# Kernel tuning notes

Hardware: AMD Instinct MI355X
Metric: run time of the kernel (lower is better)

Reference implementation:

```python
import jax, jax.numpy as jnp
import numpy as np

B, T, C = 4, 4096, 256

def setup_inputs() -> dict:
    key = jax.random.key(0)
    ks = jax.random.split(key, 7)
    s = 1.0 / np.sqrt(C)
    return {
        "x": jax.random.normal(ks[0], (B, T, C), dtype=jnp.float32),
        "Wq": jax.random.uniform(ks[1], (C, C), jnp.float32, -s, s),
        "bq": jax.random.uniform(ks[2], (C,), jnp.float32, -s, s),
        "Wk": jax.random.uniform(ks[3], (C, C), jnp.float32, -s, s),
        "bk": jax.random.uniform(ks[4], (C,), jnp.float32, -s, s),
        "Wv": jax.random.uniform(ks[5], (C, C), jnp.float32, -s, s),
        "bv": jax.random.uniform(ks[6], (C,), jnp.float32, -s, s),
    }

def reference(x, Wq, bq, Wk, bk, Wv, bv):
    # Projections (torch Linear: y = x @ W^T + b; here W stored as [in,out])
    q = x @ Wq + bq  # [B,T,C]
    k = x @ Wk + bk
    v = x @ Wv + bv
    dk = q.shape[-1]
    scores = jnp.einsum('btc,bsc->bts', q, k) / jnp.sqrt(jnp.float32(dk))
    Tn = x.shape[1]
    causal = jnp.tril(jnp.ones((Tn, Tn), dtype=bool))  # [T,T]
    scores = jnp.where(causal[None, :, :], scores, jnp.float32(-1e9))
    attn = jax.nn.softmax(scores, axis=-1)
    return jnp.einsum('bts,bsc->btc', attn, v)
```

## Files before the change

### kernel.cpp

```cpp
#include <hip/hip_runtime.h>
#include <hip/hip_bf16.h>

#define T_SEQ 4096
#define DIM   256
#define NBATCH 4

typedef short s8v __attribute__((ext_vector_type(8)));
typedef float f4v __attribute__((ext_vector_type(4)));
typedef unsigned short u16;

#define MFMA16(a,b,c) __builtin_amdgcn_mfma_f32_16x16x32_bf16(a,b,c,0,0,0)
#define FENCE_LGKM() asm volatile("s_waitcnt lgkmcnt(0)" ::: "memory")

__device__ int g_cnt[4];

static __device__ __forceinline__ u16 f2bf(float f) {
  union { float f; unsigned int u; } c; c.f = f;
  unsigned int u = c.u;
  unsigned int r = (u + 0x7fffu + ((u >> 16) & 1u)) >> 16;
  return (u16)r;
}

static __device__ __forceinline__ s8v pack8(const float* p) {
  float4 a = *(const float4*)p;
  float4 b = *(const float4*)(p + 4);
  s8v r;
  r[0] = (short)f2bf(a.x); r[1] = (short)f2bf(a.y);
  r[2] = (short)f2bf(a.z); r[3] = (short)f2bf(a.w);
  r[4] = (short)f2bf(b.x); r[5] = (short)f2bf(b.y);
  r[6] = (short)f2bf(b.z); r[7] = (short)f2bf(b.w);
  return r;
}

__global__ void diag_fill_kernel(float* __restrict__ out, float val, int n) {
  int i = blockIdx.x * blockDim.x + threadIdx.x;
  if (i < n) out[i] = val;
}

__global__ void wtrans_kernel(const float* __restrict__ Wq, const float* __restrict__ Wk,
                              const float* __restrict__ Wv, u16* __restrict__ Wt) {
  if (blockIdx.x == 0 && blockIdx.y == 0 && blockIdx.z == 0 &&
      threadIdx.y == 0 && threadIdx.x < 4)
    g_cnt[threadIdx.x] = 0;
  __shared__ float tile[32][33];
  int m = blockIdx.z;
  const float* W = (m == 0) ? Wq : ((m == 1) ? Wk : Wv);
  int bx = blockIdx.x * 32, by = blockIdx.y * 32;
  int x = threadIdx.x, y = threadIdx.y;
  #pragma unroll
  for (int i = 0; i < 32; i += 8) tile[y + i][x] = W[(by + y + i) * DIM + bx + x];
  __syncthreads();
  u16* o = Wt + m * DIM * DIM;
  #pragma unroll
  for (int i = 0; i < 32; i += 8) o[(bx + y + i) * DIM + by + x] = f2bf(tile[x][y + i]);
}

__global__ __launch_bounds__(256) void proj_kernel(
    const float* __restrict__ x, const u16* __restrict__ Wt,
    const float* __restrict__ bk, const float* __restrict__ bv,
    u16* __restrict__ kf, u16* __restrict__ vf) {
  alignas(16) __shared__ u16 Kl[64 * 264];
  alignas(16) __shared__ u16 Vl[256 * 72];

  int bid = blockIdx.x;
  int which = blockIdx.y;
  int tid  = threadIdx.x;
  int wave = tid >> 6, lane = tid & 63, quad = lane >> 4, l16 = lane & 15;
  int row0 = bid * 64 + wave * 16;

  s8v a[8];
  const float* xp = x + (size_t)(row0 + l16) * DIM + quad * 8;
  #pragma unroll
  for (int ks = 0; ks < 8; ks++) a[ks] = pack8(xp + ks * 32);

  if (which == 0) {
    const u16* W = Wt + DIM * DIM;
    f4v acc[16];
    #pragma unroll
    for (int nt = 0; nt < 16; nt++) acc[nt] = (f4v){0.f, 0.f, 0.f, 0.f};
    #pragma unroll
    for (int ks = 0; ks < 8; ks++) {
      #pragma unroll
      for (int nt = 0; nt < 16; nt++) {
        s8v bfr = *(const s8v*)(W + (nt * 16 + l16) * DIM + ks * 32 + quad * 8);
        acc[nt] = MFMA16(a[ks], bfr, acc[nt]);
      }
    }
    #pragma unroll
    for (int nt = 0; nt < 16; nt++) {
      float bb = bk[nt * 16 + l16];
      #pragma unroll
      for (int r = 0; r < 4; r++)
        Kl[(wave * 16 + quad * 4 + r) * 264 + nt * 16 + l16] = f2bf(acc[nt][r] + bb);
    }
    __syncthreads();
    #pragma unroll
    for (int i = 0; i < 8; i++) {
      int o = tid + i * 256;
      int tile = o >> 10, rem = o & 1023;
      int f = rem >> 6, ln = rem & 63;
      int sl = tile * 32 + (f >> 3) * 16 + (ln & 15);
      int c  = (f & 7) * 32 + (ln >> 4) * 8;
      s8v v = *(const s8v*)&Kl[sl * 264 + c];
      *(s8v*)&kf[(((size_t)(bid * 2 + tile) * 16 + f) * 64 + ln) * 8] = v;
    }
  } else {
    const u16* W = Wt + 2 * DIM * DIM;
    f4v acc[16];
    #pragma unroll
    for (int nt = 0; nt < 16; nt++) acc[nt] = (f4v){0.f, 0.f, 0.f, 0.f};
    #pragma unroll
    for (int ks = 0; ks < 8; ks++) {
      #pragma unroll
      for (int nt = 0; nt < 16; nt++) {
        s8v bfr = *(const s8v*)(W + (nt * 16 + l16) * DIM + ks * 32 + quad * 8);
        acc[nt] = MFMA16(a[ks], bfr, acc[nt]);
      }
    }
    #pragma unroll
    for (int nt = 0; nt < 16; nt++) {
      float bb = bv[nt * 16 + l16];
      union { u16 h[4]; uint2 v2; } pk;
      #pragma unroll
      for (int r = 0; r < 4; r++) pk.h[r] = f2bf(acc[nt][r] + bb);
      *(uint2*)&Vl[(nt * 16 + l16) * 72 + wave * 16 + quad * 4] = pk.v2;
    }
    __syncthreads();
    #pragma unroll
    for (int i = 0; i < 8; i++) {
      int o = tid + i * 256;
      int tile = o >> 10, rem = o & 1023;
      int nt = rem >> 6, ln = rem & 63;
      int c  = nt * 16 + (ln & 15);
      int sl = tile * 32 + (ln >> 4) * 8;
      s8v v = *(const s8v*)&Vl[c * 72 + sl];
      *(s8v*)&vf[(((size_t)(bid * 2 + tile) * 16 + nt) * 64 + ln) * 8] = v;
    }
  }
}

__global__ __launch_bounds__(256, 2) void attn_kernel(
    const float* __restrict__ x, const u16* __restrict__ wtq, const float* __restrict__ bq,
    const u16* __restrict__ kf, const u16* __restrict__ vf, float* __restrict__ out) {
  alignas(16) __shared__ u16 Qs[16 * 264];
  alignas(16) __shared__ float ObA[16 * 258];
  alignas(16) __shared__ float ObB[16 * 258];
  alignas(16) __shared__ u16 Ps[4 * 640];
  __shared__ float lbuf[4][16];
  __shared__ int taskS;

  int bid = blockIdx.x;
  int b = bid & 3;
  int tid = threadIdx.x;
  int wave = tid >> 6, lane = tid & 63, quad = lane >> 4, l16 = lane & 15;

  const u16* kfb = kf + (size_t)b * 128 * 8192;
  const u16* vfb = vf + (size_t)b * 128 * 8192;

  for (;;) {
    if (tid == 0) taskS = atomicAdd(&g_cnt[b], 1);
    __syncthreads();
    int t = taskS;
    if (t >= 256) break;
    int q = 255 - t;
    int row0 = q * 16;

    {
      s8v xa[8];
      const float* xp = x + (size_t)(b * T_SEQ + row0 + l16) * DIM + quad * 8;
      #pragma unroll
      for (int ks = 0; ks < 8; ks++) xa[ks] = pack8(xp + ks * 32);
      f4v qacc[4];
      #pragma unroll
      for (int j = 0; j < 4; j++) qacc[j] = (f4v){0.f, 0.f, 0.f, 0.f};
      #pragma unroll
      for (int ks = 0; ks < 8; ks++) {
        #pragma unroll
        for (int j = 0; j < 4; j++) {
          int nt = wave * 4 + j;
          s8v bfr = *(const s8v*)(wtq + (nt * 16 + l16) * DIM + ks * 32 + quad * 8);
          qacc[j] = MFMA16(xa[ks], bfr, qacc[j]);
        }
      }
      #pragma unroll
      for (int j = 0; j < 4; j++) {
        int nt = wave * 4 + j;
        float bb = bq[nt * 16 + l16];
        #pragma unroll
        for (int r = 0; r < 4; r++)
          Qs[(quad * 4 + r) * 264 + nt * 16 + l16] =
              f2bf((qacc[j][r] + bb) * 0.0625f);
      }
    }
    __syncthreads();
    s8v qa[8];
    #pragma unroll
    for (int ks = 0; ks < 8; ks++)
      qa[ks] = *(const s8v*)&Qs[l16 * 264 + ks * 32 + quad * 8];

    int n = (q >> 1) + 1;
    int lo = (n * wave) >> 2, hi = (n * (wave + 1)) >> 2;

    f4v o[16];
    #pragma unroll
    for (int nt = 0; nt < 16; nt++) o[nt] = (f4v){0.f, 0.f, 0.f, 0.f};
    float lrow[4] = {0.f, 0.f, 0.f, 0.f};

    #pragma unroll 1
    for (int kv = lo; kv < hi; kv++) {
      const u16* kt = kfb + (size_t)kv * 8192;
      const u16* vt = vfb + (size_t)kv * 8192;
      s8v kfr0[8], kfr1[8];
      #pragma unroll
      for (int f = 0; f < 8; f++) kfr0[f] = *(const s8v*)(kt + (f * 64 + lane) * 8);
      #pragma unroll
      for (int f = 0; f < 8; f++) kfr1[f] = *(const s8v*)(kt + ((8 + f) * 64 + lane) * 8);

      f4v c0 = (f4v){0.f, 0.f, 0.f, 0.f}, c1 = (f4v){0.f, 0.f, 0.f, 0.f};
      #pragma unroll
      for (int ks = 0; ks < 8; ks++) c0 = MFMA16(qa[ks], kfr0[ks], c0);
      s8v vfr0[8];
      #pragma unroll
      for (int f = 0; f < 8; f++) vfr0[f] = *(const s8v*)(vt + (f * 64 + lane) * 8);
      #pragma unroll
      for (int ks = 0; ks < 8; ks++) c1 = MFMA16(qa[ks], kfr1[ks], c1);
      s8v vfr1[8];
      #pragma unroll
      for (int f = 0; f < 8; f++) vfr1[f] = *(const s8v*)(vt + ((8 + f) * 64 + lane) * 8);

      int s0 = kv * 32 + l16;
      #pragma unroll
      for (int r = 0; r < 4; r++) {
        int tq = row0 + quad * 4 + r;
        float v0 = (s0 > tq)      ? -1e30f : c0[r];
        float v1 = (s0 + 16 > tq) ? -1e30f : c1[r];
        float p0 = __expf(v0);
        float p1 = __expf(v1);
        Ps[wave * 640 + (quad * 4 + r) * 40 + l16]      = f2bf(p0);
        Ps[wave * 640 + (quad * 4 + r) * 40 + 16 + l16] = f2bf(p1);
        lrow[r] += p0 + p1;
      }
      FENCE_LGKM();
      s8v pa = *(const s8v*)&Ps[wave * 640 + l16 * 40 + quad * 8];
      #pragma unroll
      for (int nt = 0; nt < 8; nt++) o[nt] = MFMA16(pa, vfr0[nt], o[nt]);
      #pragma unroll
      for (int nt = 0; nt < 8; nt++) o[8 + nt] = MFMA16(pa, vfr1[nt], o[8 + nt]);
    }

    #pragma unroll
    for (int r = 0; r < 4; r++) {
      #pragma unroll
      for (int d = 1; d < 16; d <<= 1) lrow[r] += __shfl_xor(lrow[r], d);
    }
    if (l16 == 0) {
      #pragma unroll
      for (int r = 0; r < 4; r++) lbuf[wave][quad * 4 + r] = lrow[r];
    }

    float* Obw = (wave & 1) ? ObB : ObA;
    if (wave < 2) {
      #pragma unroll
      for (int nt = 0; nt < 16; nt++) {
        #pragma unroll
        for (int r = 0; r < 4; r++)
          Obw[(quad * 4 + r) * 258 + nt * 16 + l16] = o[nt][r];
      }
    }
    __syncthreads();
    if (wave >= 2) {
      #pragma unroll
      for (int nt = 0; nt < 16; nt++) {
        #pragma unroll
        for (int r = 0; r < 4; r++)
          Obw[(quad * 4 + r) * 258 + nt * 16 + l16] += o[nt][r];
      }
    }
    __syncthreads();
    #pragma unroll
    for (int row = 0; row < 16; row++) {
      float s = lbuf[0][row] + lbuf[1][row] + lbuf[2][row] + lbuf[3][row];
      out[((size_t)(b * T_SEQ + row0 + row)) * DIM + tid] =
          (ObA[row * 258 + tid] + ObB[row * 258 + tid]) * (1.0f / s);
    }
  }
}

extern "C" void kernel_launch(void* const* d_in, const int* in_sizes, int n_in,
                              void* d_out, int out_size, void* d_ws, size_t ws_size,
                              hipStream_t stream) {
  const float* x  = (const float*)d_in[0];
  const float* Wq = (const float*)d_in[1];
  const float* bq = (const float*)d_in[2];
  const float* Wk = (const float*)d_in[3];
  const float* bk = (const float*)d_in[4];
  const float* Wv = (const float*)d_in[5];
  const float* bv = (const float*)d_in[6];

  const size_t NTD = (size_t)NBATCH * T_SEQ * DIM;
  const size_t WT_ELEMS = (size_t)3 * DIM * DIM;
  const size_t REQ_BYTES = (WT_ELEMS + 2 * NTD) * sizeof(u16);

  if (ws_size < REQ_BYTES) {
    float val = (float)(ws_size >> 20);
    diag_fill_kernel<<<(out_size + 255) / 256, 256, 0, stream>>>((float*)d_out, val, out_size);
    return;
  }

  u16* ws = (u16*)d_ws;
  u16* WT = ws;
  u16* Kf = ws + WT_ELEMS;
  u16* Vf = Kf + NTD;

  wtrans_kernel<<<dim3(8, 8, 3), dim3(32, 8, 1), 0, stream>>>(Wq, Wk, Wv, WT);
  proj_kernel<<<dim3(256, 2, 1), dim3(256, 1, 1), 0, stream>>>(x, WT, bk, bv, Kf, Vf);
  attn_kernel<<<dim3(512, 1, 1), dim3(256, 1, 1), 0, stream>>>(x, WT, bq, Kf, Vf, (float*)d_out);
}
```

Baseline: 220.8 us.

## Share K/V tiles in LDS across waves and split KV range with atomic accumulation

```diff
diff --git a/kernel.cpp b/kernel.cpp
--- a/kernel.cpp
+++ b/kernel.cpp
@@ -139,20 +139,27 @@
   }
 }
 
+__global__ void zero_kernel(float* __restrict__ out, float* __restrict__ lsum,
+                            int nOut, int nL) {
+  int i = blockIdx.x * blockDim.x + threadIdx.x;
+  int stride = gridDim.x * blockDim.x;
+  for (int k = i; k < nOut; k += stride) out[k] = 0.f;
+  for (int k = i; k < nL; k += stride) lsum[k] = 0.f;
+}
+
 __global__ __launch_bounds__(256, 2) void attn_kernel(
     const float* __restrict__ x, const u16* __restrict__ wtq, const float* __restrict__ bq,
-    const u16* __restrict__ kf, const u16* __restrict__ vf, float* __restrict__ out) {
-  alignas(16) __shared__ u16 Qs[16 * 264];
-  alignas(16) __shared__ float ObA[16 * 258];
-  alignas(16) __shared__ float ObB[16 * 258];
+    const u16* __restrict__ kf, const u16* __restrict__ vf,
+    float* __restrict__ lsum, float* __restrict__ out) {
+  alignas(16) __shared__ u16 KV[2][16384];
   alignas(16) __shared__ u16 Ps[4 * 640];
-  __shared__ float lbuf[4][16];
   __shared__ int taskS;
+  u16* Qs = &KV[0][0];
 
   int bid = blockIdx.x;
   int b = bid & 3;
   int tid = threadIdx.x;
-  int wave = tid >> 6, lane = tid & 63, quad = lane >> 4, l16 = lane & 15;
+  int w = tid >> 6, lane = tid & 63, quad = lane >> 4, l16 = lane & 15;
 
   const u16* kfb = kf + (size_t)b * 128 * 8192;
   const u16* vfb = vf + (size_t)b * 128 * 8192;
@@ -162,90 +169,140 @@
     __syncthreads();
     int t = taskS;
     if (t >= 256) break;
-    int q = 255 - t;
-    int row0 = q * 16;
+    int q64 = 63 - (t >> 2);
+    int qi  = t & 3;
+    int row0 = q64 * 64;
+    int n = 2 * q64 + 2;
+    int lo = (n * qi) >> 2, hi = (n * (qi + 1)) >> 2;
+    if (lo >= hi) continue;
 
     {
-      s8v xa[8];
-      const float* xp = x + (size_t)(b * T_SEQ + row0 + l16) * DIM + quad * 8;
-      #pragma unroll
-      for (int ks = 0; ks < 8; ks++) xa[ks] = pack8(xp + ks * 32);
-      f4v qacc[4];
-      #pragma unroll
-      for (int j = 0; j < 4; j++) qacc[j] = (f4v){0.f, 0.f, 0.f, 0.f};
+      f4v qacc[4][4];
+      #pragma unroll
+      for (int g = 0; g < 4; g++)
+        #pragma unroll
+        for (int j = 0; j < 4; j++) qacc[g][j] = (f4v){0.f, 0.f, 0.f, 0.f};
       #pragma unroll
       for (int ks = 0; ks < 8; ks++) {
-        #pragma unroll
-        for (int j = 0; j < 4; j++) {
-          int nt = wave * 4 + j;
-          s8v bfr = *(const s8v*)(wtq + (nt * 16 + l16) * DIM + ks * 32 + quad * 8);
-          qacc[j] = MFMA16(xa[ks], bfr, qacc[j]);
+        s8v wf[4];
+        #pragma unroll
+        for (int j = 0; j < 4; j++)
+          wf[j] = *(const s8v*)(wtq + ((w * 4 + j) * 16 + l16) * DIM + ks * 32 + quad * 8);
+        #pragma unroll
+        for (int g = 0; g < 4; g++) {
+          s8v xa = pack8(x + (size_t)(b * T_SEQ + row0 + g * 16 + l16) * DIM + ks * 32 + quad * 8);
+          #pragma unroll
+          for (int j = 0; j < 4; j++) qacc[g][j] = MFMA16(xa, wf[j], qacc[g][j]);
         }
       }
       #pragma unroll
       for (int j = 0; j < 4; j++) {
-        int nt = wave * 4 + j;
+        int nt = w * 4 + j;
         float bb = bq[nt * 16 + l16];
         #pragma unroll
-        for (int r = 0; r < 4; r++)
-          Qs[(quad * 4 + r) * 264 + nt * 16 + l16] =
-              f2bf((qacc[j][r] + bb) * 0.0625f);
+        for (int g = 0; g < 4; g++)
+          #pragma unroll
+          for (int r = 0; r < 4; r++)
+            Qs[(g * 16 + quad * 4 + r) * 264 + nt * 16 + l16] =
+                f2bf((qacc[g][j][r] + bb) * 0.0625f);
       }
     }
     __syncthreads();
     s8v qa[8];
     #pragma unroll
     for (int ks = 0; ks < 8; ks++)
-      qa[ks] = *(const s8v*)&Qs[l16 * 264 + ks * 32 + quad * 8];
-
-    int n = (q >> 1) + 1;
-    int lo = (n * wave) >> 2, hi = (n * (wave + 1)) >> 2;
+      qa[ks] = *(const s8v*)&Qs[(w * 16 + l16) * 264 + ks * 32 + quad * 8];
+    __syncthreads();
+
+    int rowBase = row0 + w * 16;
 
     f4v o[16];
     #pragma unroll
     for (int nt = 0; nt < 16; nt++) o[nt] = (f4v){0.f, 0.f, 0.f, 0.f};
     float lrow[4] = {0.f, 0.f, 0.f, 0.f};
 
+    uint4 st[8];
+    {
+      const u16* kp = kfb + ((size_t)lo << 13) + (w << 11) + (lane << 3);
+      const u16* vp = vfb + ((size_t)lo << 13) + (w << 11) + (lane << 3);
+      #pragma unroll
+      for (int i = 0; i < 4; i++) {
+        st[i]     = *(const uint4*)(kp + (i << 9));
+        st[4 + i] = *(const uint4*)(vp + (i << 9));
+      }
+      u16* kd = &KV[0][(w << 11) + (lane << 3)];
+      #pragma unroll
+      for (int i = 0; i < 4; i++) {
+        *(uint4*)(kd + (i << 9))        = st[i];
+        *(uint4*)(kd + 8192 + (i << 9)) = st[4 + i];
+      }
+    }
+    __syncthreads();
+
     #pragma unroll 1
     for (int kv = lo; kv < hi; kv++) {
-      const u16* kt = kfb + (size_t)kv * 8192;
-      const u16* vt = vfb + (size_t)kv * 8192;
-      s8v kfr0[8], kfr1[8];
-      #pragma unroll
-      for (int f = 0; f < 8; f++) kfr0[f] = *(const s8v*)(kt + (f * 64 + lane) * 8);
-      #pragma unroll
-      for (int f = 0; f < 8; f++) kfr1[f] = *(const s8v*)(kt + ((8 + f) * 64 + lane) * 8);
+      int cur = (kv - lo) & 1;
+      bool more = (kv + 1 < hi);
+
+      if (more) {
+        const u16* kp = kfb + ((size_t)(kv + 1) << 13) + (w << 11) + (lane << 3);
+        const u16* vp = vfb + ((size_t)(kv + 1) << 13) + (w << 11) + (lane << 3);
+        #pragma unroll
+        for (int i = 0; i < 4; i++) {
+          st[i]     = *(const uint4*)(kp + (i << 9));
+          st[4 + i] = *(const uint4*)(vp + (i << 9));
+        }
+      }
 
       f4v c0 = (f4v){0.f, 0.f, 0.f, 0.f}, c1 = (f4v){0.f, 0.f, 0.f, 0.f};
-      #pragma unroll
-      for (int ks = 0; ks < 8; ks++) c0 = MFMA16(qa[ks], kfr0[ks], c0);
-      s8v vfr0[8];
-      #pragma unroll
-      for (int f = 0; f < 8; f++) vfr0[f] = *(const s8v*)(vt + (f * 64 + lane) * 8);
-      #pragma unroll
-      for (int ks = 0; ks < 8; ks++) c1 = MFMA16(qa[ks], kfr1[ks], c1);
-      s8v vfr1[8];
-      #pragma unroll
-      for (int f = 0; f < 8; f++) vfr1[f] = *(const s8v*)(vt + ((8 + f) * 64 + lane) * 8);
+      {
+        s8v kfr[8];
+        #pragma unroll
+        for (int f = 0; f < 8; f++) kfr[f] = *(const s8v*)&KV[cur][(f << 9) + (lane << 3)];
+        #pragma unroll
+        for (int ks = 0; ks < 8; ks++) c0 = MFMA16(qa[ks], kfr[ks], c0);
+        #pragma unroll
+        for (int f = 0; f < 8; f++) kfr[f] = *(const s8v*)&KV[cur][((8 + f) << 9) + (lane << 3)];
+        #pragma unroll
+        for (int ks = 0; ks < 8; ks++) c1 = MFMA16(qa[ks], kfr[ks], c1);
+      }
 
       int s0 = kv * 32 + l16;
       #pragma unroll
       for (int r = 0; r < 4; r++) {
-        int tq = row0 + quad * 4 + r;
+        int tq = rowBase + quad * 4 + r;
         float v0 = (s0 > tq)      ? -1e30f : c0[r];
         float v1 = (s0 + 16 > tq) ? -1e30f : c1[r];
         float p0 = __expf(v0);
         float p1 = __expf(v1);
-        Ps[wave * 640 + (quad * 4 + r) * 40 + l16]      = f2bf(p0);
-        Ps[wave * 640 + (quad * 4 + r) * 40 + 16 + l16] = f2bf(p1);
+        Ps[w * 640 + (quad * 4 + r) * 40 + l16]      = f2bf(p0);
+        Ps[w * 640 + (quad * 4 + r) * 40 + 16 + l16] = f2bf(p1);
         lrow[r] += p0 + p1;
       }
       FENCE_LGKM();
-      s8v pa = *(const s8v*)&Ps[wave * 640 + l16 * 40 + quad * 8];
-      #pragma unroll
-      for (int nt = 0; nt < 8; nt++) o[nt] = MFMA16(pa, vfr0[nt], o[nt]);
-      #pragma unroll
-      for (int nt = 0; nt < 8; nt++) o[8 + nt] = MFMA16(pa, vfr1[nt], o[8 + nt]);
+      s8v pa = *(const s8v*)&Ps[w * 640 + l16 * 40 + quad * 8];
+
+      {
+        s8v vfr[8];
+        #pragma unroll
+        for (int f = 0; f < 8; f++) vfr[f] = *(const s8v*)&KV[cur][8192 + (f << 9) + (lane << 3)];
+        #pragma unroll
+        for (int nt = 0; nt < 8; nt++) o[nt] = MFMA16(pa, vfr[nt], o[nt]);
+        #pragma unroll
+        for (int f = 0; f < 8; f++) vfr[f] = *(const s8v*)&KV[cur][8192 + ((8 + f) << 9) + (lane << 3)];
+        #pragma unroll
+        for (int nt = 0; nt < 8; nt++) o[8 + nt] = MFMA16(pa, vfr[nt], o[8 + nt]);
+      }
+
+      if (more) {
+        u16* kd = &KV[cur ^ 1][(w << 11) + (lane << 3)];
+        #pragma unroll
+        for (int i = 0; i < 4; i++) {
+          *(uint4*)(kd + (i << 9))        = st[i];
+          *(uint4*)(kd + 8192 + (i << 9)) = st[4 + i];
+        }
+      }
+      __syncthreads();
     }
 
     #pragma unroll
@@ -255,35 +312,22 @@
     }
     if (l16 == 0) {
       #pragma unroll
-      for (int r = 0; r < 4; r++) lbuf[wave][quad * 4 + r] = lrow[r];
-    }
-
-    float* Obw = (wave & 1) ? ObB : ObA;
-    if (wave < 2) {
-      #pragma unroll
-      for (int nt = 0; nt < 16; nt++) {
-        #pragma unroll
-        for (int r = 0; r < 4; r++)
-          Obw[(quad * 4 + r) * 258 + nt * 16 + l16] = o[nt][r];
-      }
-    }
-    __syncthreads();
-    if (wave >= 2) {
-      #pragma unroll
-      for (int nt = 0; nt < 16; nt++) {
-        #pragma unroll
-        for (int r = 0; r < 4; r++)
-          Obw[(quad * 4 + r) * 258 + nt * 16 + l16] += o[nt][r];
-      }
-    }
-    __syncthreads();
-    #pragma unroll
-    for (int row = 0; row < 16; row++) {
-      float s = lbuf[0][row] + lbuf[1][row] + lbuf[2][row] + lbuf[3][row];
-      out[((size_t)(b * T_SEQ + row0 + row)) * DIM + tid] =
-          (ObA[row * 258 + tid] + ObB[row * 258 + tid]) * (1.0f / s);
+      for (int r = 0; r < 4; r++)
+        atomicAdd(&lsum[b * T_SEQ + rowBase + quad * 4 + r], lrow[r]);
+    }
+    #pragma unroll
+    for (int nt = 0; nt < 16; nt++) {
+      #pragma unroll
+      for (int r = 0; r < 4; r++)
+        atomicAdd(&out[(size_t)(b * T_SEQ + rowBase + quad * 4 + r) * DIM + nt * 16 + l16],
+                  o[nt][r]);
     }
   }
+}
+
+__global__ void norm_kernel(float* __restrict__ out, const float* __restrict__ lsum, int n) {
+  int i = blockIdx.x * blockDim.x + threadIdx.x;
+  if (i < n) out[i] *= (1.0f / lsum[i >> 8]);
 }
 
 extern "C" void kernel_launch(void* const* d_in, const int* in_sizes, int n_in,
@@ -311,8 +355,14 @@
   u16* WT = ws;
   u16* Kf = ws + WT_ELEMS;
   u16* Vf = Kf + NTD;
+  float* lsum = (float*)(ws + 2 * (size_t)DIM * DIM);
+
+  const int nOut = NBATCH * T_SEQ * DIM;
+  const int nL   = NBATCH * T_SEQ;
 
   wtrans_kernel<<<dim3(8, 8, 3), dim3(32, 8, 1), 0, stream>>>(Wq, Wk, Wv, WT);
   proj_kernel<<<dim3(256, 2, 1), dim3(256, 1, 1), 0, stream>>>(x, WT, bk, bv, Kf, Vf);
-  attn_kernel<<<dim3(512, 1, 1), dim3(256, 1, 1), 0, stream>>>(x, WT, bq, Kf, Vf, (float*)d_out);
-}
+  zero_kernel<<<2048, 256, 0, stream>>>((float*)d_out, lsum, nOut, nL);
+  attn_kernel<<<dim3(512, 1, 1), dim3(256, 1, 1), 0, stream>>>(x, WT, bq, Kf, Vf, lsum, (float*)d_out);
+  norm_kernel<<<(nOut + 255) / 256, 256, 0, stream>>>((float*)d_out, lsum, nOut);
+}
```

Result: slower. 339.6 us (+53.8%).
